# Optimization experiments

Measured on AMD Instinct MI355X. Metric: run time of the kernel, lower is better.

## Reference

```python
import jax, jax.numpy as jnp
import numpy as np

N, C, K, M = 100000, 128, 27, 4  # voxels, channels, 3^3 kernel offsets, branches
EPS = 1e-5


def setup_inputs() -> dict:
    key = jax.random.key(0)
    ks = jax.random.split(key, 4)
    x = jax.random.normal(ks[0], (N, C), jnp.float32)
    # neighbor index per voxel per kernel offset (Minkowski kernel map)
    nbr_idx = jax.random.randint(ks[1], (N, K), 0, N, dtype=jnp.int32)
    W1 = jax.random.normal(ks[2], (M, C, C), jnp.float32) * (1.0 / np.sqrt(C))
    g1 = jnp.ones((M, C), jnp.float32)
    b1 = jnp.zeros((M, C), jnp.float32)
    wk = jax.random.normal(ks[3], (M, K, C), jnp.float32) * (1.0 / np.sqrt(K))
    g_out = jnp.ones((C,), jnp.float32)
    b_out = jnp.zeros((C,), jnp.float32)
    return {"x": x, "nbr_idx": nbr_idx, "W1": W1, "g1": g1, "b1": b1,
            "wk": wk, "g_out": g_out, "b_out": b_out}


def _bn(h, g, b):
    # training-mode batch norm over the voxel axis
    mu = h.mean(0)
    var = h.var(0)
    return (h - mu) * jax.lax.rsqrt(var + EPS) * g + b


def reference(x, nbr_idx, W1, g1, b1, wk, g_out, b_out):
    out = jnp.zeros_like(x)
    for m in range(M):  # fixed small branch count
        # Conv1x1 (pointwise) + BN + ReLU
        h = jax.nn.relu(_bn(x @ W1[m], g1[m], b1[m]))  # [N, C]
        # channelwise 3^3 sparse conv: gather neighbor, per-channel scale, accumulate
        acc = jnp.zeros_like(h)
        for k in range(K):  # fixed 27 kernel offsets; avoids [N,K,C] materialization
            acc = acc + h[nbr_idx[:, k]] * wk[m, k]
        out = out + acc  # stack(-1).sum(-1) over branches
    out = jax.nn.relu(_bn(out, g_out, b_out))  # out_bn_relu
    out = out + x  # residual (inplanes == planes)
    return jax.nn.relu(out)  # final nonlinearity ('ReLU')
```

## Files before the change

### kernel.cpp

```cpp
#include <hip/hip_runtime.h>

#define KK 27
#define EPSV 1e-5f

typedef __attribute__((ext_vector_type(8))) short bf16x8;
typedef __attribute__((ext_vector_type(4))) float f32x4;
typedef __attribute__((ext_vector_type(4))) unsigned int u32x4;

static __device__ __forceinline__ unsigned short f2bf(float f) {
    unsigned u = __float_as_uint(f);
    u = u + 0x7fffu + ((u >> 16) & 1u);
    return (unsigned short)(u >> 16);
}

static __device__ __forceinline__ unsigned short f2h(float f) {
    _Float16 h = (_Float16)f;
    unsigned short u;
    __builtin_memcpy(&u, &h, 2);
    return u;
}
static __device__ __forceinline__ float h2f(unsigned short s) {
    _Float16 h;
    __builtin_memcpy(&h, &s, 2);
    return (float)h;
}
static __device__ __forceinline__ float hlo(unsigned u) { return h2f((unsigned short)(u & 0xffffu)); }
static __device__ __forceinline__ float hhi(unsigned u) { return h2f((unsigned short)(u >> 16)); }

__global__ void k0_wt(const float* __restrict__ W1, unsigned short* __restrict__ WT) {
    int m = blockIdx.x >> 7, n = blockIdx.x & 127, k = threadIdx.x;
    WT[((m * 128 + n) * 128) + k] = f2bf(W1[(m * 128 + k) * 128 + n]);
}

__launch_bounds__(256)
__global__ void kA_gemm(const float* __restrict__ x, const unsigned short* __restrict__ WT,
                        unsigned short* __restrict__ Yall, float* __restrict__ ysum,
                        float* __restrict__ ysq, int N, int m0, int m1, int ystride) {
    __shared__ unsigned short As[64 * 136];
    __shared__ unsigned short Bs[128 * 136];
    const int t = threadIdx.x;
    const int i0 = blockIdx.x * 64;

#pragma unroll
    for (int it = 0; it < 8; ++it) {
        int flat = it * 256 + t;
        int r = flat >> 5, c4 = (flat & 31) * 4;
        float4 v = make_float4(0.f, 0.f, 0.f, 0.f);
        if (i0 + r < N) v = *(const float4*)(x + (size_t)(i0 + r) * 128 + c4);
        ushort4 bb;
        bb.x = f2bf(v.x); bb.y = f2bf(v.y); bb.z = f2bf(v.z); bb.w = f2bf(v.w);
        *(ushort4*)(As + r * 136 + c4) = bb;
    }

    const int w = t >> 6, lane = t & 63;
    const int wr = w >> 1, wc = w & 1;
    const int r16 = lane & 15, q = lane >> 4;

    for (int m = m0; m < m1; ++m) {
        __syncthreads();
        const uint4* Wp = (const uint4*)(WT + (size_t)m * 128 * 128);
#pragma unroll
        for (int it = 0; it < 8; ++it) {
            int flat = it * 256 + t;
            int n = flat >> 4, kc = flat & 15;
            uint4 v = Wp[n * 16 + kc];
            *(uint4*)(Bs + n * 136 + kc * 8) = v;
        }
        __syncthreads();

        f32x4 acc[2][4];
#pragma unroll
        for (int a = 0; a < 2; ++a)
#pragma unroll
            for (int b = 0; b < 4; ++b) { acc[a][b][0] = 0.f; acc[a][b][1] = 0.f; acc[a][b][2] = 0.f; acc[a][b][3] = 0.f; }

#pragma unroll
        for (int ks = 0; ks < 4; ++ks) {
            int ko = ks * 32 + q * 8;
            bf16x8 af[2], bfr[4];
#pragma unroll
            for (int ri = 0; ri < 2; ++ri)
                af[ri] = *(const bf16x8*)(As + (wr * 32 + ri * 16 + r16) * 136 + ko);
#pragma unroll
            for (int ci = 0; ci < 4; ++ci)
                bfr[ci] = *(const bf16x8*)(Bs + (wc * 64 + ci * 16 + r16) * 136 + ko);
#pragma unroll
            for (int ri = 0; ri < 2; ++ri)
#pragma unroll
                for (int ci = 0; ci < 4; ++ci)
                    acc[ri][ci] = __builtin_amdgcn_mfma_f32_16x16x32_bf16(af[ri], bfr[ci], acc[ri][ci], 0, 0, 0);
        }

#pragma unroll
        for (int ci = 0; ci < 4; ++ci) {
            float s = 0.f, s2 = 0.f;
#pragma unroll
            for (int ri = 0; ri < 2; ++ri) {
#pragma unroll
                for (int r = 0; r < 4; ++r) {
                    int row = i0 + wr * 32 + ri * 16 + q * 4 + r;
                    float vv = acc[ri][ci][r];
                    if (row < N) { s += vv; s2 += vv * vv; }
                }
            }
            s  += __shfl_xor(s, 16);  s  += __shfl_xor(s, 32);
            s2 += __shfl_xor(s2, 16); s2 += __shfl_xor(s2, 32);
            if (lane < 16) {
                int col = wc * 64 + ci * 16 + r16;
                atomicAdd(ysum + m * 128 + col, s);
                atomicAdd(ysq  + m * 128 + col, s2);
            }
        }

        __syncthreads();
        unsigned short* Ys = Bs;
#pragma unroll
        for (int ci = 0; ci < 4; ++ci) {
            int col = wc * 64 + ci * 16 + r16;
#pragma unroll
            for (int ri = 0; ri < 2; ++ri) {
#pragma unroll
                for (int r = 0; r < 4; ++r) {
                    int rl = wr * 32 + ri * 16 + q * 4 + r;
                    Ys[rl * 136 + col] = f2h(acc[ri][ci][r]);
                }
            }
        }
        __syncthreads();
        const int cb = (m - m0) * 128;
#pragma unroll
        for (int it = 0; it < 4; ++it) {
            int chunk = it * 256 + t;
            int row = chunk >> 4, c8 = (chunk & 15) * 8;
            if (i0 + row < N) {
                u32x4 v = *(const u32x4*)(Ys + row * 136 + c8);
                __builtin_nontemporal_store(v, (u32x4*)(Yall + (size_t)(i0 + row) * ystride + cb + c8));
            }
        }
    }
}

__global__ void k2_coef(const float* __restrict__ ysum, const float* __restrict__ ysq,
                        const float* __restrict__ g1, const float* __restrict__ b1,
                        float* __restrict__ a1, float* __restrict__ c1, int N, int m0) {
    int c = threadIdx.x & 127;
    int m = m0 + (threadIdx.x >> 7);
    float mean = ysum[m * 128 + c] / (float)N;
    float var  = ysq[m * 128 + c] / (float)N - mean * mean;
    float a = g1[m * 128 + c] * rsqrtf(var + EPSV);
    a1[m * 128 + c] = a;
    c1[m * 128 + c] = b1[m * 128 + c] - mean * a;
}

__launch_bounds__(256)
__global__ void kH_bn(unsigned short* __restrict__ Y, const float* __restrict__ a1,
                      const float* __restrict__ c1, int N) {
    long long i = (long long)blockIdx.x * 256 + threadIdx.x;
    if (i >= (long long)N * 64) return;
    const int e0 = ((int)i & 63) * 8;
    uint4 v = *(const uint4*)(Y + (i << 3));
    const float4 A0 = *(const float4*)(a1 + e0);
    const float4 A1 = *(const float4*)(a1 + e0 + 4);
    const float4 C0 = *(const float4*)(c1 + e0);
    const float4 C1 = *(const float4*)(c1 + e0 + 4);
    float h0 = fmaxf(0.f, hlo(v.x) * A0.x + C0.x);
    float h1 = fmaxf(0.f, hhi(v.x) * A0.y + C0.y);
    float h2 = fmaxf(0.f, hlo(v.y) * A0.z + C0.z);
    float h3 = fmaxf(0.f, hhi(v.y) * A0.w + C0.w);
    float h4 = fmaxf(0.f, hlo(v.z) * A1.x + C1.x);
    float h5 = fmaxf(0.f, hhi(v.z) * A1.y + C1.y);
    float h6 = fmaxf(0.f, hlo(v.w) * A1.z + C1.z);
    float h7 = fmaxf(0.f, hhi(v.w) * A1.w + C1.w);
    uint4 o;
    o.x = (unsigned)f2h(h0) | ((unsigned)f2h(h1) << 16);
    o.y = (unsigned)f2h(h2) | ((unsigned)f2h(h3) << 16);
    o.z = (unsigned)f2h(h4) | ((unsigned)f2h(h5) << 16);
    o.w = (unsigned)f2h(h6) | ((unsigned)f2h(h7) << 16);
    *(uint4*)(Y + (i << 3)) = o;
}

__launch_bounds__(256)
__global__ void k4_all(const unsigned short* __restrict__ H, const int* __restrict__ nbr,
                       const float* __restrict__ wkg, float* __restrict__ P,
                       float* __restrict__ osum, float* __restrict__ osq, int N) {
    __shared__ unsigned short wkL[4 * KK * 136];
    __shared__ float ssum[128], ssq[128];
    const int t = threadIdx.x;
    for (int idx = t; idx < 4 * KK * 128; idx += 256) {
        int c = idx & 127, km = idx >> 7;
        wkL[km * 136 + c] = f2h(wkg[idx]);
    }
    if (t < 128) { ssum[t] = 0.f; ssq[t] = 0.f; }
    __syncthreads();

    const int lane = t & 63;
    const int m = lane >> 4, c16 = lane & 15;
    const unsigned short* wbase = wkL + (m * KK) * 136 + c16 * 8;
    const unsigned short* hbase = H + lane * 8;

    float os[8], oq[8];
#pragma unroll
    for (int e = 0; e < 8; ++e) { os[e] = 0.f; oq[e] = 0.f; }

    const int wid = blockIdx.x * 4 + (t >> 6);
    const int nw  = gridDim.x * 4;
    const int npair = (N + 1) >> 1;
    for (int vp = wid; vp < npair; vp += nw) {
        const int v0 = __builtin_amdgcn_readfirstlane(vp * 2);
        const bool has1 = (v0 + 1) < N;
        const int* np0 = nbr + (size_t)v0 * KK;
        const int* np1 = np0 + (has1 ? KK : 0);
        float acc0[8], acc1[8];
#pragma unroll
        for (int e = 0; e < 8; ++e) { acc0[e] = 0.f; acc1[e] = 0.f; }

#pragma unroll 3
        for (int k = 0; k < KK; ++k) {
            const int j0 = np0[k];
            const int j1 = np1[k];
            const uint4 h0v = *(const uint4*)(hbase + ((size_t)j0 << 9));
            const uint4 h1v = *(const uint4*)(hbase + ((size_t)j1 << 9));
            const uint4 wv  = *(const uint4*)(wbase + k * 136);
            const float w0 = hlo(wv.x), w1 = hhi(wv.x), w2 = hlo(wv.y), w3 = hhi(wv.y);
            const float w4 = hlo(wv.z), w5 = hhi(wv.z), w6 = hlo(wv.w), w7 = hhi(wv.w);
            acc0[0] += hlo(h0v.x) * w0; acc0[1] += hhi(h0v.x) * w1;
            acc0[2] += hlo(h0v.y) * w2; acc0[3] += hhi(h0v.y) * w3;
            acc0[4] += hlo(h0v.z) * w4; acc0[5] += hhi(h0v.z) * w5;
            acc0[6] += hlo(h0v.w) * w6; acc0[7] += hhi(h0v.w) * w7;
            acc1[0] += hlo(h1v.x) * w0; acc1[1] += hhi(h1v.x) * w1;
            acc1[2] += hlo(h1v.y) * w2; acc1[3] += hhi(h1v.y) * w3;
            acc1[4] += hlo(h1v.z) * w4; acc1[5] += hhi(h1v.z) * w5;
            acc1[6] += hlo(h1v.w) * w6; acc1[7] += hhi(h1v.w) * w7;
        }

#pragma unroll
        for (int e = 0; e < 8; ++e) {
            acc0[e] += __shfl_xor(acc0[e], 16);
            acc0[e] += __shfl_xor(acc0[e], 32);
            acc1[e] += __shfl_xor(acc1[e], 16);
            acc1[e] += __shfl_xor(acc1[e], 32);
        }
        const int q = lane >> 4;
        if (q == 0 || (q == 1 && has1)) {
            float av[8];
#pragma unroll
            for (int e = 0; e < 8; ++e) av[e] = (q == 0) ? acc0[e] : acc1[e];
            f32x4 x0 = {av[0], av[1], av[2], av[3]};
            f32x4 x1 = {av[4], av[5], av[6], av[7]};
            float* p = P + (size_t)(v0 + q) * 128 + c16 * 8;
            __builtin_nontemporal_store(x0, (f32x4*)p);
            __builtin_nontemporal_store(x1, (f32x4*)(p + 4));
#pragma unroll
            for (int e = 0; e < 8; ++e) { os[e] += av[e]; oq[e] += av[e] * av[e]; }
        }
    }

    if ((lane >> 4) < 2) {
#pragma unroll
        for (int e = 0; e < 8; ++e) {
            atomicAdd(ssum + c16 * 8 + e, os[e]);
            atomicAdd(ssq  + c16 * 8 + e, oq[e]);
        }
    }
    __syncthreads();
    if (t < 128) {
        atomicAdd(osum + t, ssum[t]);
        atomicAdd(osq  + t, ssq[t]);
    }
}

template <int MODE>
__launch_bounds__(256)
__global__ void k4_gather(const unsigned short* __restrict__ Ym, int ystride,
                          const int* __restrict__ nbr,
                          const float* __restrict__ wkm, const float* __restrict__ a1m,
                          const float* __restrict__ c1m, float* __restrict__ P,
                          float* __restrict__ osum, float* __restrict__ osq, int N) {
    __shared__ float wkL[KK * 132];
    __shared__ float ssum[128], ssq[128];
    const int t = threadIdx.x;
    for (int idx = t; idx < KK * 128; idx += 256) {
        int k = idx >> 7, c = idx & 127;
        wkL[k * 132 + c] = wkm[k * 128 + c];
    }
    if (MODE == 2) { if (t < 128) { ssum[t] = 0.f; ssq[t] = 0.f; } }

    const int w = t >> 6, lane = t & 63;
    const int q = lane >> 4, c16 = lane & 15;
    const int slot = w * 4 + q;
    const int vox = blockIdx.x * 16 + slot;
    const bool alive = vox < N;

    float aR[8], cR[8];
    {
        const float4 A0 = *(const float4*)(a1m + c16 * 8);
        const float4 A1 = *(const float4*)(a1m + c16 * 8 + 4);
        const float4 C0 = *(const float4*)(c1m + c16 * 8);
        const float4 C1 = *(const float4*)(c1m + c16 * 8 + 4);
        aR[0]=A0.x; aR[1]=A0.y; aR[2]=A0.z; aR[3]=A0.w;
        aR[4]=A1.x; aR[5]=A1.y; aR[6]=A1.z; aR[7]=A1.w;
        cR[0]=C0.x; cR[1]=C0.y; cR[2]=C0.z; cR[3]=C0.w;
        cR[4]=C1.x; cR[5]=C1.y; cR[6]=C1.z; cR[7]=C1.w;
    }
    __syncthreads();

    const long long base = alive ? (long long)vox * KK : 0;
    float acc[8];
#pragma unroll
    for (int e = 0; e < 8; ++e) acc[e] = 0.f;

#pragma unroll 3
    for (int k = 0; k < KK; ++k) {
        int j = nbr[base + k];
        const uint4 hv = *(const uint4*)(Ym + (size_t)j * ystride + c16 * 8);
        const float4 wa = *(const float4*)(wkL + k * 132 + c16 * 8);
        const float4 wb = *(const float4*)(wkL + k * 132 + c16 * 8 + 4);
        float h0 = fmaxf(0.f, hlo(hv.x) * aR[0] + cR[0]);
        float h1 = fmaxf(0.f, hhi(hv.x) * aR[1] + cR[1]);
        float h2 = fmaxf(0.f, hlo(hv.y) * aR[2] + cR[2]);
        float h3 = fmaxf(0.f, hhi(hv.y) * aR[3] + cR[3]);
        float h4 = fmaxf(0.f, hlo(hv.z) * aR[4] + cR[4]);
        float h5 = fmaxf(0.f, hhi(hv.z) * aR[5] + cR[5]);
        float h6 = fmaxf(0.f, hlo(hv.w) * aR[6] + cR[6]);
        float h7 = fmaxf(0.f, hhi(hv.w) * aR[7] + cR[7]);
        acc[0] += h0 * wa.x; acc[1] += h1 * wa.y;
        acc[2] += h2 * wa.z; acc[3] += h3 * wa.w;
        acc[4] += h4 * wb.x; acc[5] += h5 * wb.y;
        acc[6] += h6 * wb.z; acc[7] += h7 * wb.w;
    }

    float os[8], oq[8];
    if (alive) {
        float* p = P + (size_t)vox * 128 + c16 * 8;
        if (MODE == 0) {
            float4 v0 = {acc[0], acc[1], acc[2], acc[3]};
            float4 v1 = {acc[4], acc[5], acc[6], acc[7]};
            *(float4*)p = v0;
            *(float4*)(p + 4) = v1;
        } else {
            float4 o0 = *(const float4*)p, o1 = *(const float4*)(p + 4);
            o0.x += acc[0]; o0.y += acc[1]; o0.z += acc[2]; o0.w += acc[3];
            o1.x += acc[4]; o1.y += acc[5]; o1.z += acc[6]; o1.w += acc[7];
            *(float4*)p = o0;
            *(float4*)(p + 4) = o1;
            if (MODE == 2) {
                os[0] = o0.x; oq[0] = o0.x * o0.x;
                os[1] = o0.y; oq[1] = o0.y * o0.y;
                os[2] = o0.z; oq[2] = o0.z * o0.z;
                os[3] = o0.w; oq[3] = o0.w * o0.w;
                os[4] = o1.x; oq[4] = o1.x * o1.x;
                os[5] = o1.y; oq[5] = o1.y * o1.y;
                os[6] = o1.z; oq[6] = o1.z * o1.z;
                os[7] = o1.w; oq[7] = o1.w * o1.w;
            }
        }
    }
    if (MODE == 2) {
        if (!alive) {
#pragma unroll
            for (int e = 0; e < 8; ++e) { os[e] = 0.f; oq[e] = 0.f; }
        }
#pragma unroll
        for (int e = 0; e < 8; ++e) {
            os[e] += __shfl_xor(os[e], 16); os[e] += __shfl_xor(os[e], 32);
            oq[e] += __shfl_xor(oq[e], 16); oq[e] += __shfl_xor(oq[e], 32);
        }
        if (lane < 16) {
#pragma unroll
            for (int e = 0; e < 8; ++e) {
                atomicAdd(ssum + c16 * 8 + e, os[e]);
                atomicAdd(ssq  + c16 * 8 + e, oq[e]);
            }
        }
        __syncthreads();
        if (t < 128) {
            atomicAdd(osum + t, ssum[t]);
            atomicAdd(osq  + t, ssq[t]);
        }
    }
}

__global__ void k5_coef(const float* __restrict__ osum, const float* __restrict__ osq,
                        const float* __restrict__ g, const float* __restrict__ b,
                        float* __restrict__ ao, float* __restrict__ co, int N) {
    int c = threadIdx.x;
    float mean = osum[c] / (float)N;
    float var  = osq[c] / (float)N - mean * mean;
    float a = g[c] * rsqrtf(var + EPSV);
    ao[c] = a;
    co[c] = b[c] - mean * a;
}

__launch_bounds__(256)
__global__ void k6_final(float* __restrict__ P, const float* __restrict__ x,
                         const float* __restrict__ ao, const float* __restrict__ co, int N) {
    long long t4 = ((long long)blockIdx.x * 256 + threadIdx.x) * 4;
    if (t4 >= (long long)N * 128) return;
    int c4 = (int)(t4 & 127);
    float4 p  = *(const float4*)(P + t4);
    float4 xv = *(const float4*)(x + t4);
    float4 a  = *(const float4*)(ao + c4);
    float4 c  = *(const float4*)(co + c4);
    float4 o;
    o.x = fmaxf(0.f, fmaxf(0.f, p.x * a.x + c.x) + xv.x);
    o.y = fmaxf(0.f, fmaxf(0.f, p.y * a.y + c.y) + xv.y);
    o.z = fmaxf(0.f, fmaxf(0.f, p.z * a.z + c.z) + xv.z);
    o.w = fmaxf(0.f, fmaxf(0.f, p.w * a.w + c.w) + xv.w);
    *(float4*)(P + t4) = o;
}

extern "C" void kernel_launch(void* const* d_in, const int* in_sizes, int n_in,
                              void* d_out, int out_size, void* d_ws, size_t ws_size,
                              hipStream_t stream) {
    const float* x     = (const float*)d_in[0];
    const int*   nbr   = (const int*)d_in[1];
    const float* W1    = (const float*)d_in[2];
    const float* g1    = (const float*)d_in[3];
    const float* b1    = (const float*)d_in[4];
    const float* wk    = (const float*)d_in[5];
    const float* g_out = (const float*)d_in[6];
    const float* b_out = (const float*)d_in[7];
    const int N = in_sizes[0] / 128;

    float* P = (float*)d_out;
    char* ws = (char*)d_ws;
    float* ysum = (float*)ws;
    float* ysq  = ysum + 512;
    float* osum = ysq + 512;
    float* osq  = osum + 128;
    float* a1   = osq + 128;
    float* c1   = a1 + 512;
    float* ao   = c1 + 512;
    float* co   = ao + 128;
    unsigned short* WT = (unsigned short*)(ws + 16384);
    unsigned short* Y  = (unsigned short*)(ws + 16384 + 131072);

    const bool fused = ws_size >= (size_t)16384 + 131072 + (size_t)N * 512 * 2;

    hipMemsetAsync(d_ws, 0, 5120, stream);
    k0_wt<<<512, 128, 0, stream>>>(W1, WT);

    const int gA = (N + 63) / 64;
    const int g4 = (N + 15) / 16;

    if (fused) {
        kA_gemm<<<gA, 256, 0, stream>>>(x, WT, Y, ysum, ysq, N, 0, 4, 512);
        k2_coef<<<1, 512, 0, stream>>>(ysum, ysq, g1, b1, a1, c1, N, 0);
        const long long chunks = (long long)N * 64;
        const int gH = (int)((chunks + 255) / 256);
        kH_bn<<<gH, 256, 0, stream>>>(Y, a1, c1, N);
        k4_all<<<2048, 256, 0, stream>>>(Y, nbr, wk, P, osum, osq, N);
    } else {
        for (int m = 0; m < 4; ++m) {
            kA_gemm<<<gA, 256, 0, stream>>>(x, WT, Y, ysum, ysq, N, m, m + 1, 128);
            k2_coef<<<1, 128, 0, stream>>>(ysum, ysq, g1, b1, a1, c1, N, m);
            if (m == 0)
                k4_gather<0><<<g4, 256, 0, stream>>>(Y, 128, nbr, wk + m * KK * 128,
                                                     a1 + m * 128, c1 + m * 128, P, osum, osq, N);
            else if (m == 3)
                k4_gather<2><<<g4, 256, 0, stream>>>(Y, 128, nbr, wk + m * KK * 128,
                                                     a1 + m * 128, c1 + m * 128, P, osum, osq, N);
            else
                k4_gather<1><<<g4, 256, 0, stream>>>(Y, 128, nbr, wk + m * KK * 128,
                                                     a1 + m * 128, c1 + m * 128, P, osum, osq, N);
        }
    }
    k5_coef<<<1, 128, 0, stream>>>(osum, osq, g_out, b_out, ao, co, N);
    const int g6 = (int)(((long long)N * 128 / 4 + 255) / 256);
    k6_final<<<g6, 256, 0, stream>>>(P, x, ao, co, N);
}
```

Baseline: 660.2 us.

## Split neighbor gather into source-range slices to improve cache locality

The gather over all branches is now done in four passes, each touching only neighbors whose index falls in one quarter of the voxel range, so each pass's working set of H is a quarter as large and fits better in L2/MALL. Partial sums go to P and are read back and re-accumulated in later passes, and BN statistics are taken only in the final pass. In exchange, the neighbor indices are re-read four times, the inner loop gains divergent branches, and P sees several extra read-modify-write passes.

```diff
diff --git a/kernel.cpp b/kernel.cpp
--- a/kernel.cpp
+++ b/kernel.cpp
@@ -2,6 +2,7 @@
 
 #define KK 27
 #define EPSV 1e-5f
+#define NSLICE 4
 
 typedef __attribute__((ext_vector_type(8))) short bf16x8;
 typedef __attribute__((ext_vector_type(4))) float f32x4;
@@ -195,6 +196,7 @@
 
     const int lane = t & 63;
     const int m = lane >> 4, c16 = lane & 15;
+    const int q = lane >> 4;
     const unsigned short* wbase = wkL + (m * KK) * 136 + c16 * 8;
     const unsigned short* hbase = H + lane * 8;
 
@@ -205,57 +207,77 @@
     const int wid = blockIdx.x * 4 + (t >> 6);
     const int nw  = gridDim.x * 4;
     const int npair = (N + 1) >> 1;
-    for (int vp = wid; vp < npair; vp += nw) {
-        const int v0 = __builtin_amdgcn_readfirstlane(vp * 2);
-        const bool has1 = (v0 + 1) < N;
-        const int* np0 = nbr + (size_t)v0 * KK;
-        const int* np1 = np0 + (has1 ? KK : 0);
-        float acc0[8], acc1[8];
-#pragma unroll
-        for (int e = 0; e < 8; ++e) { acc0[e] = 0.f; acc1[e] = 0.f; }
+    const int slen = (N + NSLICE - 1) / NSLICE;
+
+    for (int pass = 0; pass < NSLICE; ++pass) {
+        const int lo = pass * slen, hi = lo + slen;
+        for (int vp = wid; vp < npair; vp += nw) {
+            const int v0 = __builtin_amdgcn_readfirstlane(vp * 2);
+            const bool has1 = (v0 + 1) < N;
+            const int* np0 = nbr + (size_t)v0 * KK;
+            const int* np1 = np0 + (has1 ? KK : 0);
+            float acc0[8], acc1[8];
+#pragma unroll
+            for (int e = 0; e < 8; ++e) { acc0[e] = 0.f; acc1[e] = 0.f; }
 
 #pragma unroll 3
-        for (int k = 0; k < KK; ++k) {
-            const int j0 = np0[k];
-            const int j1 = np1[k];
-            const uint4 h0v = *(const uint4*)(hbase + ((size_t)j0 << 9));
-            const uint4 h1v = *(const uint4*)(hbase + ((size_t)j1 << 9));
-            const uint4 wv  = *(const uint4*)(wbase + k * 136);
-            const float w0 = hlo(wv.x), w1 = hhi(wv.x), w2 = hlo(wv.y), w3 = hhi(wv.y);
-            const float w4 = hlo(wv.z), w5 = hhi(wv.z), w6 = hlo(wv.w), w7 = hhi(wv.w);
-            acc0[0] += hlo(h0v.x) * w0; acc0[1] += hhi(h0v.x) * w1;
-            acc0[2] += hlo(h0v.y) * w2; acc0[3] += hhi(h0v.y) * w3;
-            acc0[4] += hlo(h0v.z) * w4; acc0[5] += hhi(h0v.z) * w5;
-            acc0[6] += hlo(h0v.w) * w6; acc0[7] += hhi(h0v.w) * w7;
-            acc1[0] += hlo(h1v.x) * w0; acc1[1] += hhi(h1v.x) * w1;
-            acc1[2] += hlo(h1v.y) * w2; acc1[3] += hhi(h1v.y) * w3;
-            acc1[4] += hlo(h1v.z) * w4; acc1[5] += hhi(h1v.z) * w5;
-            acc1[6] += hlo(h1v.w) * w6; acc1[7] += hhi(h1v.w) * w7;
-        }
-
-#pragma unroll
-        for (int e = 0; e < 8; ++e) {
-            acc0[e] += __shfl_xor(acc0[e], 16);
-            acc0[e] += __shfl_xor(acc0[e], 32);
-            acc1[e] += __shfl_xor(acc1[e], 16);
-            acc1[e] += __shfl_xor(acc1[e], 32);
-        }
-        const int q = lane >> 4;
-        if (q == 0 || (q == 1 && has1)) {
-            float av[8];
-#pragma unroll
-            for (int e = 0; e < 8; ++e) av[e] = (q == 0) ? acc0[e] : acc1[e];
-            f32x4 x0 = {av[0], av[1], av[2], av[3]};
-            f32x4 x1 = {av[4], av[5], av[6], av[7]};
-            float* p = P + (size_t)(v0 + q) * 128 + c16 * 8;
-            __builtin_nontemporal_store(x0, (f32x4*)p);
-            __builtin_nontemporal_store(x1, (f32x4*)(p + 4));
-#pragma unroll
-            for (int e = 0; e < 8; ++e) { os[e] += av[e]; oq[e] += av[e] * av[e]; }
-        }
-    }
-
-    if ((lane >> 4) < 2) {
+            for (int k = 0; k < KK; ++k) {
+                const int j0 = np0[k];
+                const int j1 = np1[k];
+                const bool in0 = (j0 >= lo) & (j0 < hi);
+                const bool in1 = (j1 >= lo) & (j1 < hi);
+                if (in0 | in1) {
+                    const uint4 wv = *(const uint4*)(wbase + k * 136);
+                    const float w0 = hlo(wv.x), w1 = hhi(wv.x), w2 = hlo(wv.y), w3 = hhi(wv.y);
+                    const float w4 = hlo(wv.z), w5 = hhi(wv.z), w6 = hlo(wv.w), w7 = hhi(wv.w);
+                    if (in0) {
+                        const uint4 hv = *(const uint4*)(hbase + ((size_t)j0 << 9));
+                        acc0[0] += hlo(hv.x) * w0; acc0[1] += hhi(hv.x) * w1;
+                        acc0[2] += hlo(hv.y) * w2; acc0[3] += hhi(hv.y) * w3;
+                        acc0[4] += hlo(hv.z) * w4; acc0[5] += hhi(hv.z) * w5;
+                        acc0[6] += hlo(hv.w) * w6; acc0[7] += hhi(hv.w) * w7;
+                    }
+                    if (in1) {
+                        const uint4 hv = *(const uint4*)(hbase + ((size_t)j1 << 9));
+                        acc1[0] += hlo(hv.x) * w0; acc1[1] += hhi(hv.x) * w1;
+                        acc1[2] += hlo(hv.y) * w2; acc1[3] += hhi(hv.y) * w3;
+                        acc1[4] += hlo(hv.z) * w4; acc1[5] += hhi(hv.z) * w5;
+                        acc1[6] += hlo(hv.w) * w6; acc1[7] += hhi(hv.w) * w7;
+                    }
+                }
+            }
+
+#pragma unroll
+            for (int e = 0; e < 8; ++e) {
+                acc0[e] += __shfl_xor(acc0[e], 16);
+                acc0[e] += __shfl_xor(acc0[e], 32);
+                acc1[e] += __shfl_xor(acc1[e], 16);
+                acc1[e] += __shfl_xor(acc1[e], 32);
+            }
+            if (q == 0 || (q == 1 && has1)) {
+                float av[8];
+#pragma unroll
+                for (int e = 0; e < 8; ++e) av[e] = (q == 0) ? acc0[e] : acc1[e];
+                float* p = P + (size_t)(v0 + q) * 128 + c16 * 8;
+                if (pass > 0) {
+                    f32x4 o0 = __builtin_nontemporal_load((const f32x4*)p);
+                    f32x4 o1 = __builtin_nontemporal_load((const f32x4*)(p + 4));
+                    av[0] += o0[0]; av[1] += o0[1]; av[2] += o0[2]; av[3] += o0[3];
+                    av[4] += o1[0]; av[5] += o1[1]; av[6] += o1[2]; av[7] += o1[3];
+                }
+                f32x4 x0 = {av[0], av[1], av[2], av[3]};
+                f32x4 x1 = {av[4], av[5], av[6], av[7]};
+                __builtin_nontemporal_store(x0, (f32x4*)p);
+                __builtin_nontemporal_store(x1, (f32x4*)(p + 4));
+                if (pass == NSLICE - 1) {
+#pragma unroll
+                    for (int e = 0; e < 8; ++e) { os[e] += av[e]; oq[e] += av[e] * av[e]; }
+                }
+            }
+        }
+    }
+
+    if (q < 2) {
 #pragma unroll
         for (int e = 0; e < 8; ++e) {
             atomicAdd(ssum + c16 * 8 + e, os[e]);
```

Measured after the change: 779.0 us. 18.0% more time.

## Fuse BN+ReLU into gather kernel and process four voxels per wave

Applied to the files above, without the earlier changes.

Removes the separate kH_bn pass that rewrote the fp16 pre-activation buffer in place. The BN affine and ReLU are now applied to each gathered neighbor value inside k4_all, using per-lane scale and shift held in registers. The gather loop also handles four voxels per wave instead of two, so all four 16-lane groups write output and contribute to the statistics. This saves a full read-write pass over the N×512 buffer. In exchange, the BN arithmetic is repeated 27 times per value and the wider unroll raises register pressure.

```diff
diff --git a/kernel.cpp b/kernel.cpp
--- a/kernel.cpp
+++ b/kernel.cpp
@@ -153,35 +153,9 @@
 }
 
 __launch_bounds__(256)
-__global__ void kH_bn(unsigned short* __restrict__ Y, const float* __restrict__ a1,
-                      const float* __restrict__ c1, int N) {
-    long long i = (long long)blockIdx.x * 256 + threadIdx.x;
-    if (i >= (long long)N * 64) return;
-    const int e0 = ((int)i & 63) * 8;
-    uint4 v = *(const uint4*)(Y + (i << 3));
-    const float4 A0 = *(const float4*)(a1 + e0);
-    const float4 A1 = *(const float4*)(a1 + e0 + 4);
-    const float4 C0 = *(const float4*)(c1 + e0);
-    const float4 C1 = *(const float4*)(c1 + e0 + 4);
-    float h0 = fmaxf(0.f, hlo(v.x) * A0.x + C0.x);
-    float h1 = fmaxf(0.f, hhi(v.x) * A0.y + C0.y);
-    float h2 = fmaxf(0.f, hlo(v.y) * A0.z + C0.z);
-    float h3 = fmaxf(0.f, hhi(v.y) * A0.w + C0.w);
-    float h4 = fmaxf(0.f, hlo(v.z) * A1.x + C1.x);
-    float h5 = fmaxf(0.f, hhi(v.z) * A1.y + C1.y);
-    float h6 = fmaxf(0.f, hlo(v.w) * A1.z + C1.z);
-    float h7 = fmaxf(0.f, hhi(v.w) * A1.w + C1.w);
-    uint4 o;
-    o.x = (unsigned)f2h(h0) | ((unsigned)f2h(h1) << 16);
-    o.y = (unsigned)f2h(h2) | ((unsigned)f2h(h3) << 16);
-    o.z = (unsigned)f2h(h4) | ((unsigned)f2h(h5) << 16);
-    o.w = (unsigned)f2h(h6) | ((unsigned)f2h(h7) << 16);
-    *(uint4*)(Y + (i << 3)) = o;
-}
-
-__launch_bounds__(256)
-__global__ void k4_all(const unsigned short* __restrict__ H, const int* __restrict__ nbr,
-                       const float* __restrict__ wkg, float* __restrict__ P,
+__global__ void k4_all(const unsigned short* __restrict__ Y, const int* __restrict__ nbr,
+                       const float* __restrict__ wkg, const float* __restrict__ A1g,
+                       const float* __restrict__ C1g, float* __restrict__ P,
                        float* __restrict__ osum, float* __restrict__ osq, int N) {
     __shared__ unsigned short wkL[4 * KK * 136];
     __shared__ float ssum[128], ssq[128];
@@ -191,12 +165,25 @@
         wkL[km * 136 + c] = f2h(wkg[idx]);
     }
     if (t < 128) { ssum[t] = 0.f; ssq[t] = 0.f; }
-    __syncthreads();
 
     const int lane = t & 63;
     const int m = lane >> 4, c16 = lane & 15;
+    const int q = m;
     const unsigned short* wbase = wkL + (m * KK) * 136 + c16 * 8;
-    const unsigned short* hbase = H + lane * 8;
+    const unsigned short* hbase = Y + lane * 8;
+
+    float Ar[8], Cr[8];
+    {
+        const float4 A0 = *(const float4*)(A1g + m * 128 + c16 * 8);
+        const float4 A1 = *(const float4*)(A1g + m * 128 + c16 * 8 + 4);
+        const float4 C0 = *(const float4*)(C1g + m * 128 + c16 * 8);
+        const float4 C1 = *(const float4*)(C1g + m * 128 + c16 * 8 + 4);
+        Ar[0]=A0.x; Ar[1]=A0.y; Ar[2]=A0.z; Ar[3]=A0.w;
+        Ar[4]=A1.x; Ar[5]=A1.y; Ar[6]=A1.z; Ar[7]=A1.w;
+        Cr[0]=C0.x; Cr[1]=C0.y; Cr[2]=C0.z; Cr[3]=C0.w;
+        Cr[4]=C1.x; Cr[5]=C1.y; Cr[6]=C1.z; Cr[7]=C1.w;
+    }
+    __syncthreads();
 
     float os[8], oq[8];
 #pragma unroll
@@ -204,50 +191,62 @@
 
     const int wid = blockIdx.x * 4 + (t >> 6);
     const int nw  = gridDim.x * 4;
-    const int npair = (N + 1) >> 1;
-    for (int vp = wid; vp < npair; vp += nw) {
-        const int v0 = __builtin_amdgcn_readfirstlane(vp * 2);
-        const bool has1 = (v0 + 1) < N;
-        const int* np0 = nbr + (size_t)v0 * KK;
-        const int* np1 = np0 + (has1 ? KK : 0);
-        float acc0[8], acc1[8];
-#pragma unroll
-        for (int e = 0; e < 8; ++e) { acc0[e] = 0.f; acc1[e] = 0.f; }
+    const int ng  = (N + 3) >> 2;
+    for (int vg = wid; vg < ng; vg += nw) {
+        const int v0 = __builtin_amdgcn_readfirstlane(vg << 2);
+        const int* np = nbr + (size_t)v0 * KK;
+        const int o1 = (v0 + 1 < N) ? KK : 0;
+        const int o2 = (v0 + 2 < N) ? 2 * KK : 0;
+        const int o3 = (v0 + 3 < N) ? 3 * KK : 0;
+        float acc0[8], acc1[8], acc2[8], acc3[8];
+#pragma unroll
+        for (int e = 0; e < 8; ++e) { acc0[e] = 0.f; acc1[e] = 0.f; acc2[e] = 0.f; acc3[e] = 0.f; }
 
 #pragma unroll 3
         for (int k = 0; k < KK; ++k) {
-            const int j0 = np0[k];
-            const int j1 = np1[k];
-            const uint4 h0v = *(const uint4*)(hbase + ((size_t)j0 << 9));
-            const uint4 h1v = *(const uint4*)(hbase + ((size_t)j1 << 9));
+            const int j0 = np[k];
+            const int j1 = np[o1 + k];
+            const int j2 = np[o2 + k];
+            const int j3 = np[o3 + k];
+            const uint4 hv0 = *(const uint4*)(hbase + ((size_t)j0 << 9));
+            const uint4 hv1 = *(const uint4*)(hbase + ((size_t)j1 << 9));
+            const uint4 hv2 = *(const uint4*)(hbase + ((size_t)j2 << 9));
+            const uint4 hv3 = *(const uint4*)(hbase + ((size_t)j3 << 9));
             const uint4 wv  = *(const uint4*)(wbase + k * 136);
             const float w0 = hlo(wv.x), w1 = hhi(wv.x), w2 = hlo(wv.y), w3 = hhi(wv.y);
             const float w4 = hlo(wv.z), w5 = hhi(wv.z), w6 = hlo(wv.w), w7 = hhi(wv.w);
-            acc0[0] += hlo(h0v.x) * w0; acc0[1] += hhi(h0v.x) * w1;
-            acc0[2] += hlo(h0v.y) * w2; acc0[3] += hhi(h0v.y) * w3;
-            acc0[4] += hlo(h0v.z) * w4; acc0[5] += hhi(h0v.z) * w5;
-            acc0[6] += hlo(h0v.w) * w6; acc0[7] += hhi(h0v.w) * w7;
-            acc1[0] += hlo(h1v.x) * w0; acc1[1] += hhi(h1v.x) * w1;
-            acc1[2] += hlo(h1v.y) * w2; acc1[3] += hhi(h1v.y) * w3;
-            acc1[4] += hlo(h1v.z) * w4; acc1[5] += hhi(h1v.z) * w5;
-            acc1[6] += hlo(h1v.w) * w6; acc1[7] += hhi(h1v.w) * w7;
+#define K4BODY(A, H)                                                        \
+            A[0] += fmaxf(0.f, hlo(H.x) * Ar[0] + Cr[0]) * w0;              \
+            A[1] += fmaxf(0.f, hhi(H.x) * Ar[1] + Cr[1]) * w1;              \
+            A[2] += fmaxf(0.f, hlo(H.y) * Ar[2] + Cr[2]) * w2;              \
+            A[3] += fmaxf(0.f, hhi(H.y) * Ar[3] + Cr[3]) * w3;              \
+            A[4] += fmaxf(0.f, hlo(H.z) * Ar[4] + Cr[4]) * w4;              \
+            A[5] += fmaxf(0.f, hhi(H.z) * Ar[5] + Cr[5]) * w5;              \
+            A[6] += fmaxf(0.f, hlo(H.w) * Ar[6] + Cr[6]) * w6;              \
+            A[7] += fmaxf(0.f, hhi(H.w) * Ar[7] + Cr[7]) * w7;
+            K4BODY(acc0, hv0)
+            K4BODY(acc1, hv1)
+            K4BODY(acc2, hv2)
+            K4BODY(acc3, hv3)
+#undef K4BODY
         }
 
 #pragma unroll
         for (int e = 0; e < 8; ++e) {
-            acc0[e] += __shfl_xor(acc0[e], 16);
-            acc0[e] += __shfl_xor(acc0[e], 32);
-            acc1[e] += __shfl_xor(acc1[e], 16);
-            acc1[e] += __shfl_xor(acc1[e], 32);
-        }
-        const int q = lane >> 4;
-        if (q == 0 || (q == 1 && has1)) {
-            float av[8];
-#pragma unroll
-            for (int e = 0; e < 8; ++e) av[e] = (q == 0) ? acc0[e] : acc1[e];
+            acc0[e] += __shfl_xor(acc0[e], 16); acc0[e] += __shfl_xor(acc0[e], 32);
+            acc1[e] += __shfl_xor(acc1[e], 16); acc1[e] += __shfl_xor(acc1[e], 32);
+            acc2[e] += __shfl_xor(acc2[e], 16); acc2[e] += __shfl_xor(acc2[e], 32);
+            acc3[e] += __shfl_xor(acc3[e], 16); acc3[e] += __shfl_xor(acc3[e], 32);
+        }
+        float av[8];
+#pragma unroll
+        for (int e = 0; e < 8; ++e)
+            av[e] = (q == 0) ? acc0[e] : (q == 1) ? acc1[e] : (q == 2) ? acc2[e] : acc3[e];
+        const int vq = v0 + q;
+        if (vq < N) {
             f32x4 x0 = {av[0], av[1], av[2], av[3]};
             f32x4 x1 = {av[4], av[5], av[6], av[7]};
-            float* p = P + (size_t)(v0 + q) * 128 + c16 * 8;
+            float* p = P + (size_t)vq * 128 + c16 * 8;
             __builtin_nontemporal_store(x0, (f32x4*)p);
             __builtin_nontemporal_store(x1, (f32x4*)(p + 4));
 #pragma unroll
@@ -255,12 +254,10 @@
         }
     }
 
-    if ((lane >> 4) < 2) {
-#pragma unroll
-        for (int e = 0; e < 8; ++e) {
-            atomicAdd(ssum + c16 * 8 + e, os[e]);
-            atomicAdd(ssq  + c16 * 8 + e, oq[e]);
-        }
+#pragma unroll
+    for (int e = 0; e < 8; ++e) {
+        atomicAdd(ssum + c16 * 8 + e, os[e]);
+        atomicAdd(ssq  + c16 * 8 + e, oq[e]);
     }
     __syncthreads();
     if (t < 128) {
@@ -446,10 +443,7 @@
     if (fused) {
         kA_gemm<<<gA, 256, 0, stream>>>(x, WT, Y, ysum, ysq, N, 0, 4, 512);
         k2_coef<<<1, 512, 0, stream>>>(ysum, ysq, g1, b1, a1, c1, N, 0);
-        const long long chunks = (long long)N * 64;
-        const int gH = (int)((chunks + 255) / 256);
-        kH_bn<<<gH, 256, 0, stream>>>(Y, a1, c1, N);
-        k4_all<<<2048, 256, 0, stream>>>(Y, nbr, wk, P, osum, osq, N);
+        k4_all<<<2048, 256, 0, stream>>>(Y, nbr, wk, a1, c1, P, osum, osq, N);
     } else {
         for (int m = 0; m < 4; ++m) {
             kA_gemm<<<gA, 256, 0, stream>>>(x, WT, Y, ysum, ysq, N, m, m + 1, 128);
```

Result: faster. 647.0 us (-2.0%).
